# Kernel optimization log

Hardware: AMD Instinct MI355X
Metric: run time of the kernel (lower is better)

The kernel has to match this reference:

```python
import jax, jax.numpy as jnp
import numpy as np

T, Q, D, NH, L = 6, 300, 256, 8, 4
DH = D // NH
PC, PT = 2, 1
WT = T - 1
P = PC + WT * PT
DFF = 1024
SHAPES = [(128, 128), (64, 64), (32, 32), (16, 16)]
S_PER_FRAME = sum(h * w for h, w in SHAPES)


def _layer_norm(x, g, b, eps=1e-5):
    mu = jnp.mean(x, -1, keepdims=True)
    v = jnp.mean(jnp.square(x - mu), -1, keepdims=True)
    return (x - mu) * jax.lax.rsqrt(v + eps) * g + b


def _bilinear(vlh, loc, frame_pt, Hl, Wl):
    # vlh: [NH, T*Hl*Wl, DH]; loc: [TQ, NH, P, 2] normalized; frame_pt: np [TQ, P] int32
    x = loc[..., 0] * Wl - 0.5
    y = loc[..., 1] * Hl - 0.5
    x0 = jnp.floor(x)
    y0 = jnp.floor(y)
    fx = x - x0
    fy = y - y0
    x0 = x0.astype(jnp.int32)
    y0 = y0.astype(jnp.int32)
    fbase = (frame_pt[:, None, :] * np.int32(Hl * Wl)).astype(np.int32)  # [TQ,1,P]
    acc = 0.0
    for dy, wy in ((0, 1.0 - fy), (1, fy)):
        for dx, wx in ((0, 1.0 - fx), (1, fx)):
            xi = x0 + dx
            yi = y0 + dy
            ok = (xi >= 0) & (xi < Wl) & (yi >= 0) & (yi < Hl)
            idx = fbase + jnp.clip(yi, 0, Hl - 1) * Wl + jnp.clip(xi, 0, Wl - 1)  # [TQ,NH,P]
            g = jax.vmap(lambda v, i: v[i], in_axes=(0, 1), out_axes=0)(vlh, idx)  # [NH,TQ,P,DH]
            w = wy * wx * ok  # [TQ,NH,P]
            acc = acc + g * jnp.transpose(w, (1, 0, 2))[..., None]
    return acc  # [NH,TQ,P,DH]


def _forward(src, tgt_masks, query_pos, reference_points, src_valid_ratios,
             Wq, bq, Wk, bk, Wv, bv, Wo, bo, norm2_g, norm2_b,
             Wval, bval, Woff, boff, Watt, batt, Wout, bout, norm1_g, norm1_b,
             W1, b1, W2, b2, norm3_g, norm3_b,
             src_spatial_shapes, src_level_start_index):
    shapes = np.asarray(src_spatial_shapes)
    # ---- self-attention across frames (seq=T, batch=Q, as in nn.MultiheadAttention) ----
    qk_in = tgt_masks + query_pos  # [T,Q,D]
    qh = (qk_in @ Wq.T + bq).reshape(T, Q, NH, DH)
    kh = (qk_in @ Wk.T + bk).reshape(T, Q, NH, DH)
    vh = (tgt_masks @ Wv.T + bv).reshape(T, Q, NH, DH)
    logits = jnp.einsum('iqhd,jqhd->qhij', qh, kh) * (1.0 / np.sqrt(DH))
    attn = jax.nn.softmax(logits, -1)
    sa = jnp.einsum('qhij,jqhd->iqhd', attn, vh).reshape(T, Q, D) @ Wo.T + bo
    tgt = _layer_norm(tgt_masks + sa, norm2_g, norm2_b)  # [T,Q,D]

    tgt = tgt.reshape(T * Q, D)
    query = tgt + query_pos.reshape(T * Q, D)

    # ---- current-frame and temporal (same-instance) reference points ----
    ref = reference_points.reshape(T * Q, 2)
    vr0 = src_valid_ratios[0]  # [L,2]
    ref_curr = ref[:, None, :] * vr0[None]  # [TQ,L,2]
    others = np.array([[f for f in range(T) if f != t] for t in range(T)], np.int32)  # [T,WT]
    ref_oth = reference_points[others]  # [T,WT,Q,2]
    ref_oth = jnp.transpose(ref_oth, (0, 2, 1, 3)).reshape(T * Q, WT, 2)
    ref_temp = ref_oth[:, :, None, :] * vr0[None, None]  # [TQ,WT,L,2]

    fid = np.repeat(np.arange(T, dtype=np.int32), Q)  # [TQ]
    oth_fid = np.repeat(others, Q, axis=0)  # [TQ,WT]
    frame_pt = np.concatenate([np.tile(fid[:, None], (1, PC)), oth_fid], axis=1).astype(np.int32)  # [TQ,P]

    # ---- temporal multi-scale deformable cross-attention ----
    value = (src[0] @ Wval.T + bval).reshape(-1, NH, DH)  # [T*S,NH,DH]
    off = (query @ Woff.T + boff).reshape(T * Q, NH, L, P, 2)
    att = jax.nn.softmax((query @ Watt.T + batt).reshape(T * Q, NH, L * P), -1)
    att = att.reshape(T * Q, NH, L, P)

    out = jnp.zeros((T * Q, NH, DH), src.dtype)
    start = 0
    for l in range(L):
        Hl, Wl = int(shapes[l, 0]), int(shapes[l, 1])
        n = T * Hl * Wl
        vlh = value[start:start + n].transpose(1, 0, 2)  # [NH, T*Hl*Wl, DH]
        start += n
        bc = jnp.tile(ref_curr[:, l][:, None, :], (1, PC, 1))  # [TQ,PC,2]
        bt = ref_temp[:, :, l, :]  # [TQ,WT,2]
        base = jnp.concatenate([bc, bt], 1)[:, None]  # [TQ,1,P,2]
        loc = base + off[:, :, l] / jnp.array([Wl, Hl], jnp.float32)  # [TQ,NH,P,2]
        sampled = _bilinear(vlh, loc, frame_pt, Hl, Wl)  # [NH,TQ,P,DH]
        out = out + jnp.einsum('nqpd,qnp->qnd', sampled, att[:, :, l])
    cross = out.reshape(T * Q, D) @ Wout.T + bout
    tgt = _layer_norm(tgt + cross, norm1_g, norm1_b)

    # ---- FFN ----
    h = jax.nn.relu(tgt @ W1.T + b1)
    tgt = _layer_norm(tgt + h @ W2.T + b2, norm3_g, norm3_b)
    return tgt.reshape(T, Q, D)


def setup_inputs() -> dict:
    key = jax.random.key(0)
    ki = iter(jax.random.split(key, 48))

    def rn(shape, s=1.0):
        return jax.random.normal(next(ki), shape, jnp.float32) * s

    return {
        'src': rn((1, T * S_PER_FRAME, D)),
        'tgt_masks': rn((T, Q, D)),
        'query_pos': rn((T, Q, D), 0.5),
        'reference_points': jax.random.uniform(next(ki), (T, Q, 2), jnp.float32, 0.25, 0.75),
        'src_valid_ratios': jax.random.uniform(next(ki), (T, L, 2), jnp.float32, 0.9, 1.0),
        'src_spatial_shapes': jnp.array(SHAPES, jnp.int32),
        'src_level_start_index': jnp.array(np.cumsum([0] + [T * h * w for h, w in SHAPES[:-1]]), jnp.int32),
        'Wq': rn((D, D), 0.02), 'bq': jnp.zeros((D,)),
        'Wk': rn((D, D), 0.02), 'bk': jnp.zeros((D,)),
        'Wv': rn((D, D), 0.02), 'bv': jnp.zeros((D,)),
        'Wo': rn((D, D), 0.02), 'bo': jnp.zeros((D,)),
        'norm2_g': jnp.ones((D,)), 'norm2_b': jnp.zeros((D,)),
        'Wval': rn((D, D), 0.02), 'bval': jnp.zeros((D,)),
        'Woff': rn((NH * L * P * 2, D), 0.01), 'boff': rn((NH * L * P * 2,), 0.1),
        'Watt': rn((NH * L * P, D), 0.01), 'batt': jnp.zeros((NH * L * P,)),
        'Wout': rn((D, D), 0.02), 'bout': jnp.zeros((D,)),
        'norm1_g': jnp.ones((D,)), 'norm1_b': jnp.zeros((D,)),
        'W1': rn((DFF, D), 0.02), 'b1': jnp.zeros((DFF,)),
        'W2': rn((D, DFF), 0.02), 'b2': jnp.zeros((D,)),
        'norm3_g': jnp.ones((D,)), 'norm3_b': jnp.zeros((D,)),
    }


def reference(src, tgt_masks, query_pos, reference_points, src_valid_ratios,
              src_spatial_shapes, src_level_start_index,
              Wq, bq, Wk, bk, Wv, bv, Wo, bo, norm2_g, norm2_b,
              Wval, bval, Woff, boff, Watt, batt, Wout, bout, norm1_g, norm1_b,
              W1, b1, W2, b2, norm3_g, norm3_b):
    return _forward(src, tgt_masks, query_pos, reference_points, src_valid_ratios,
                    Wq, bq, Wk, bk, Wv, bv, Wo, bo, norm2_g, norm2_b,
                    Wval, bval, Woff, boff, Watt, batt, Wout, bout, norm1_g, norm1_b,
                    W1, b1, W2, b2, norm3_g, norm3_b,
                    src_spatial_shapes, src_level_start_index)
```

## Files before the change

kernel.cpp:

```cpp
#include <hip/hip_runtime.h>
#include <hip/hip_bf16.h>

#define T_ 6
#define Q_ 300
#define TQ 1800
#define D_ 256
#define NH_ 8
#define DH_ 32
#define L_ 4
#define P_ 7
#define DFF_ 1024
#define NV 130560
#define NVB 1020
#define QKVB 174

#define OW_VAL 0
#define OW_Q   65536
#define OW_K   131072
#define OW_V   196608
#define OW_O   262144
#define OW_OUT 327680
#define OW_OFF 393216
#define OW_ATT 507904
#define OW_1   565248
#define OW_2   827392
#define OW_TOT 1089536

typedef __attribute__((ext_vector_type(8))) short bf16x8;
typedef __attribute__((ext_vector_type(4))) float f32x4;
typedef __attribute__((ext_vector_type(8))) unsigned short u16x8;
typedef __attribute__((ext_vector_type(4))) unsigned short u16x4;

__device__ inline float bf2f(unsigned short s) {
    union { unsigned u; float f; } v; v.u = ((unsigned)s) << 16;
    return v.f;
}
__device__ inline unsigned short f2b_rn(float f) {
    __hip_bfloat16 h = __float2bfloat16(f);
    union { __hip_bfloat16 h; unsigned short u; } c; c.h = h; return c.u;
}

__global__ __launch_bounds__(256) void wcvt_kernel(
    const float* __restrict__ s0, const float* __restrict__ s1,
    const float* __restrict__ s2, const float* __restrict__ s3,
    const float* __restrict__ s4, const float* __restrict__ s5,
    const float* __restrict__ s6, const float* __restrict__ s7,
    const float* __restrict__ s8, const float* __restrict__ s9,
    unsigned short* __restrict__ dst)
{
    int idx4 = blockIdx.x * blockDim.x + threadIdx.x;
    const int total4 = OW_TOT / 4;
    for (; idx4 < total4; idx4 += gridDim.x * blockDim.x) {
        int e = idx4 * 4;
        const float* s; int off;
        if      (e < OW_Q)   { s = s0; off = e; }
        else if (e < OW_K)   { s = s1; off = e - OW_Q; }
        else if (e < OW_V)   { s = s2; off = e - OW_K; }
        else if (e < OW_O)   { s = s3; off = e - OW_V; }
        else if (e < OW_OUT) { s = s4; off = e - OW_O; }
        else if (e < OW_OFF) { s = s5; off = e - OW_OUT; }
        else if (e < OW_ATT) { s = s6; off = e - OW_OFF; }
        else if (e < OW_1)   { s = s7; off = e - OW_ATT; }
        else if (e < OW_2)   { s = s8; off = e - OW_1; }
        else                 { s = s9; off = e - OW_2; }
        f32x4 v = *(const f32x4*)(s + off);
        u16x4 o;
#pragma unroll
        for (int j = 0; j < 4; j++) o[j] = f2b_rn(v[j]);
        *(u16x4*)(dst + e) = o;
    }
}

__global__ __launch_bounds__(512, 4) void mega1_kernel(
    const float* __restrict__ A, const unsigned short* __restrict__ wbf,
    const float* __restrict__ bias,
    unsigned short* __restrict__ out,
    const float* __restrict__ tgtm, const float* __restrict__ qpos,
    const float* __restrict__ bq, const float* __restrict__ bk,
    const float* __restrict__ bv,
    float* __restrict__ qh, float* __restrict__ kh, float* __restrict__ vh)
{
    __shared__ unsigned short As[2][128 * 32];
    __shared__ unsigned short Bs[2][256 * 32];

    int tid = threadIdx.x;
    int wave = tid >> 6, lane = tid & 63;
    int r = lane & 15, g = lane >> 4;

    if (blockIdx.x < NVB) {
        const unsigned short* Wv = wbf + OW_VAL;
        int wm = wave >> 2, wn = wave & 3;
        int m0 = blockIdx.x * 128;

        int arow = tid >> 2, aq = tid & 3;
        const float* aptr = A + (size_t)(m0 + arow) * 256 + aq * 8;

        int dcol = (wave * 2) * 16 + (lane >> 2);
        int dkk = (lane & 3) * 8;

        f32x4 acc[4][4] = {};
        f32x4 aLo, aHi;

#define DMA_B(ks, buf) do { \
            const unsigned short* s0_ = Wv + (size_t)dcol * 256 + (ks) * 32 + dkk; \
            const unsigned short* s1_ = s0_ + 16 * 256; \
            __builtin_amdgcn_global_load_lds( \
                (const __attribute__((address_space(1))) void*)s0_, \
                (__attribute__((address_space(3))) void*)&Bs[buf][(wave * 2 + 0) * 512], 16, 0, 0); \
            __builtin_amdgcn_global_load_lds( \
                (const __attribute__((address_space(1))) void*)s1_, \
                (__attribute__((address_space(3))) void*)&Bs[buf][(wave * 2 + 1) * 512], 16, 0, 0); \
        } while (0)

        DMA_B(0, 0);
        aLo = *(const f32x4*)(aptr);
        aHi = *(const f32x4*)(aptr + 4);

#pragma unroll
        for (int ks = 0; ks < 8; ks++) {
            const int buf = ks & 1;
            u16x8 av;
#pragma unroll
            for (int j = 0; j < 4; j++) { av[j] = f2b_rn(aLo[j]); av[4 + j] = f2b_rn(aHi[j]); }
            *(u16x8*)&As[buf][arow * 32 + aq * 8] = av;

            asm volatile("s_waitcnt lgkmcnt(0)" ::: "memory");
            __builtin_amdgcn_s_barrier();
            __builtin_amdgcn_sched_barrier(0);

            if (ks < 7) {
                DMA_B(ks + 1, buf ^ 1);
                aLo = *(const f32x4*)(aptr + (ks + 1) * 32);
                aHi = *(const f32x4*)(aptr + (ks + 1) * 32 + 4);
            }

            bf16x8 af[4], bfr[4];
#pragma unroll
            for (int mi = 0; mi < 4; mi++)
                af[mi] = *(const bf16x8*)&As[buf][(wm * 64 + mi * 16 + r) * 32 + g * 8];
#pragma unroll
            for (int ni = 0; ni < 4; ni++)
                bfr[ni] = *(const bf16x8*)&Bs[buf][(wn * 64 + ni * 16 + r) * 32 + g * 8];
#pragma unroll
            for (int mi = 0; mi < 4; mi++)
#pragma unroll
                for (int ni = 0; ni < 4; ni++)
                    acc[mi][ni] = __builtin_amdgcn_mfma_f32_16x16x32_bf16(af[mi], bfr[ni], acc[mi][ni], 0, 0, 0);
        }
#undef DMA_B

#pragma unroll
        for (int ni = 0; ni < 4; ni++) {
            int col = wn * 64 + ni * 16 + r;
            float bv2 = bias[col];
#pragma unroll
            for (int mi = 0; mi < 4; mi++) {
#pragma unroll
                for (int rr = 0; rr < 4; rr++) {
                    int row = m0 + wm * 64 + mi * 16 + g * 4 + rr;
                    out[(size_t)row * 256 + col] = f2b_rn(acc[mi][ni][rr] + bv2);
                }
            }
        }
    } else {
        int b = blockIdx.x - NVB;
        int bmx = b % 29, by = b / 29;
        int wm = wave >> 2, wn = wave & 3;
        int m0 = bmx * 64 + wm * 32;
        int n0g = by * 128 + wn * 32;
        int seg = n0g >> 8;
        int n0 = n0g & 255;
        const unsigned short* Wp = wbf + (seg == 0 ? OW_Q : (seg == 1 ? OW_K : OW_V));
        const float* bp = (seg == 0) ? bq : (seg == 1) ? bk : bv;
        float* outp = (seg == 0) ? qh : (seg == 1) ? kh : vh;
        bool add2 = (seg < 2);

        f32x4 acc[2][2] = {};
#pragma unroll
        for (int kk = 0; kk < 256; kk += 32) {
            int kbase = kk + g * 8;
            bf16x8 af[2], wf[2];
#pragma unroll
            for (int mi = 0; mi < 2; mi++) {
                int row = m0 + mi * 16 + r; if (row >= TQ) row = TQ - 1;
                const float* ap = tgtm + (size_t)row * 256 + kbase;
                f32x4 lo = *(const f32x4*)ap, hi = *(const f32x4*)(ap + 4);
                if (add2) {
                    const float* ap2 = qpos + (size_t)row * 256 + kbase;
                    lo += *(const f32x4*)ap2; hi += *(const f32x4*)(ap2 + 4);
                }
#pragma unroll
                for (int j = 0; j < 4; j++) { af[mi][j] = (short)f2b_rn(lo[j]); af[mi][4 + j] = (short)f2b_rn(hi[j]); }
            }
#pragma unroll
            for (int ni = 0; ni < 2; ni++) {
                int col = n0 + ni * 16 + r;
                wf[ni] = *(const bf16x8*)&Wp[(size_t)col * 256 + kbase];
            }
#pragma unroll
            for (int mi = 0; mi < 2; mi++)
#pragma unroll
                for (int ni = 0; ni < 2; ni++)
                    acc[mi][ni] = __builtin_amdgcn_mfma_f32_16x16x32_bf16(af[mi], wf[ni], acc[mi][ni], 0, 0, 0);
        }
#pragma unroll
        for (int mi = 0; mi < 2; mi++)
#pragma unroll
            for (int ni = 0; ni < 2; ni++) {
                int col = n0 + ni * 16 + r;
                float bv2 = bp[col];
#pragma unroll
                for (int rr = 0; rr < 4; rr++) {
                    int row = m0 + mi * 16 + g * 4 + rr;
                    if (row < TQ) outp[(size_t)row * 256 + col] = acc[mi][ni][rr] + bv2;
                }
            }
    }
}

__global__ __launch_bounds__(256) void attn_wo_ln2_kernel(
    const float* __restrict__ qh, const float* __restrict__ kh,
    const float* __restrict__ vh, const float* __restrict__ tgtm,
    const float* __restrict__ qpos, const unsigned short* __restrict__ wbf,
    const float* __restrict__ bo, const float* __restrict__ n2g,
    const float* __restrict__ n2b,
    float* __restrict__ tgt1, float* __restrict__ query)
{
    int q = blockIdx.x;
    int tid = threadIdx.x;
    __shared__ float qs[T_][D_], ks_[T_][D_], vs[T_][D_];
    __shared__ unsigned short po[16][268];
    __shared__ float sa32[16][264];

#pragma unroll
    for (int i = 0; i < T_; i++) {
        size_t base = (size_t)(i * Q_ + q) * D_ + tid;
        qs[i][tid] = qh[base]; ks_[i][tid] = kh[base]; vs[i][tid] = vh[base];
    }
    __syncthreads();

    const float scale = 0.17677669529663687f;
    float lg[T_][T_];
#pragma unroll
    for (int i = 0; i < T_; i++)
#pragma unroll
        for (int j = 0; j < T_; j++) {
            float p = qs[i][tid] * ks_[j][tid];
#pragma unroll
            for (int m = 16; m >= 1; m >>= 1) p += __shfl_xor(p, m, 32);
            lg[i][j] = p * scale;
        }
#pragma unroll
    for (int i = 0; i < T_; i++) {
        float mx = lg[i][0];
#pragma unroll
        for (int j = 1; j < T_; j++) mx = fmaxf(mx, lg[i][j]);
        float w[T_]; float sum = 0.f;
#pragma unroll
        for (int j = 0; j < T_; j++) { w[j] = __expf(lg[i][j] - mx); sum += w[j]; }
        float inv = 1.f / sum;
        float a = 0.f;
#pragma unroll
        for (int j = 0; j < T_; j++) a += w[j] * inv * vs[j][tid];
        po[i][tid] = f2b_rn(a);
    }
#pragma unroll
    for (int i = T_; i < 16; i++) po[i][tid] = 0;
    __syncthreads();

    const unsigned short* Wo = wbf + OW_O;
    int wn = tid >> 6, lane = tid & 63;
    int r = lane & 15, g = lane >> 4;
    f32x4 acc[4] = {};
#pragma unroll
    for (int ksx = 0; ksx < 8; ksx++) {
        int kbase = ksx * 32 + g * 8;
        bf16x8 af = *(const bf16x8*)&po[r][kbase];
        bf16x8 bfr[4];
#pragma unroll
        for (int ni = 0; ni < 4; ni++)
            bfr[ni] = *(const bf16x8*)&Wo[(size_t)(wn * 64 + ni * 16 + r) * 256 + kbase];
#pragma unroll
        for (int ni = 0; ni < 4; ni++)
            acc[ni] = __builtin_amdgcn_mfma_f32_16x16x32_bf16(af, bfr[ni], acc[ni], 0, 0, 0);
    }
#pragma unroll
    for (int ni = 0; ni < 4; ni++) {
        int col = wn * 64 + ni * 16 + r;
#pragma unroll
        for (int rr = 0; rr < 4; rr++) {
            int row = g * 4 + rr;
            if (row < T_)
                sa32[row][col] = acc[ni][rr] + bo[col] + tgtm[(size_t)(row * Q_ + q) * 256 + col];
        }
    }
    __syncthreads();

    int rl = tid >> 3, l8 = tid & 7;
    if (rl < T_) {
        float s = 0.f, s2 = 0.f;
#pragma unroll
        for (int c = 0; c < 256; c += 8) {
            float v = sa32[rl][c + l8];
            s += v; s2 += v * v;
        }
#pragma unroll
        for (int m = 4; m >= 1; m >>= 1) { s += __shfl_xor(s, m, 64); s2 += __shfl_xor(s2, m, 64); }
        float mu = s * (1.f / 256.f);
        float var = s2 * (1.f / 256.f) - mu * mu;
        float rs = rsqrtf(var + 1e-5f);
        size_t grow = (size_t)(rl * Q_ + q) * 256;
#pragma unroll
        for (int c = 0; c < 256; c += 8) {
            int cc = c + l8;
            float y = (sa32[rl][cc] - mu) * rs * n2g[cc] + n2b[cc];
            tgt1[grow + cc] = y;
            query[grow + cc] = y + qpos[grow + cc];
        }
    }
}

__global__ __launch_bounds__(256) void offatt_kernel(
    const float* __restrict__ query, const unsigned short* __restrict__ wbf,
    const float* __restrict__ boff, const float* __restrict__ batt,
    float* __restrict__ offb, float* __restrict__ attl)
{
    int wave = threadIdx.x >> 6;
    int lane = threadIdx.x & 63;
    int wm = wave >> 1, wn = wave & 1;
    int m0 = blockIdx.x * 64 + wm * 32;
    int n0g = blockIdx.y * 64 + wn * 32;
    int seg = (n0g >= 448);
    int n0 = seg ? (n0g - 448) : n0g;
    int Nloc = seg ? 224 : 448;
    const unsigned short* W = wbf + (seg ? OW_ATT : OW_OFF);
    const float* bias = seg ? batt : boff;
    float* out = seg ? attl : offb;
    int r = lane & 15, g = lane >> 4;

    f32x4 acc[2][2] = {};
#pragma unroll
    for (int kk = 0; kk < 256; kk += 32) {
        int kbase = kk + g * 8;
        bf16x8 af[2], wf[2];
#pragma unroll
        for (int mi = 0; mi < 2; mi++) {
            int row = m0 + mi * 16 + r; if (row >= TQ) row = TQ - 1;
            const float* ap = query + (size_t)row * 256 + kbase;
            f32x4 lo = *(const f32x4*)ap, hi = *(const f32x4*)(ap + 4);
#pragma unroll
            for (int j = 0; j < 4; j++) { af[mi][j] = (short)f2b_rn(lo[j]); af[mi][4 + j] = (short)f2b_rn(hi[j]); }
        }
#pragma unroll
        for (int ni = 0; ni < 2; ni++) {
            int col = n0 + ni * 16 + r; if (col >= Nloc) col = Nloc - 1;
            wf[ni] = *(const bf16x8*)&W[(size_t)col * 256 + kbase];
        }
#pragma unroll
        for (int mi = 0; mi < 2; mi++)
#pragma unroll
            for (int ni = 0; ni < 2; ni++)
                acc[mi][ni] = __builtin_amdgcn_mfma_f32_16x16x32_bf16(af[mi], wf[ni], acc[mi][ni], 0, 0, 0);
    }
#pragma unroll
    for (int mi = 0; mi < 2; mi++)
#pragma unroll
        for (int ni = 0; ni < 2; ni++) {
            int col = n0 + ni * 16 + r;
            if (col < Nloc) {
                float bv2 = bias[col];
#pragma unroll
                for (int rr = 0; rr < 4; rr++) {
                    int row = m0 + mi * 16 + g * 4 + rr;
                    if (row < TQ) out[(size_t)row * Nloc + col] = acc[mi][ni][rr] + bv2;
                }
            }
        }
}

__global__ __launch_bounds__(256) void sample_kernel(
    const unsigned short* __restrict__ value, const float* __restrict__ attl,
    const float* __restrict__ off, const float* __restrict__ refp,
    const float* __restrict__ vr, float* __restrict__ out)
{
    int q = blockIdx.x;
    int tid = threadIdx.x;
    int d = tid & 31, h = tid >> 5;
    int t = q / Q_, qq = q - t * Q_;

    __shared__ float aw[NH_][28], ofx[NH_][28], ofy[NH_][28];

    float lgv = (d < 28) ? attl[(size_t)q * 224 + h * 28 + d] : -1e30f;
    float mx = lgv;
#pragma unroll
    for (int m = 16; m >= 1; m >>= 1) mx = fmaxf(mx, __shfl_xor(mx, m, 32));
    float e = (d < 28) ? __expf(lgv - mx) : 0.f;
    float s = e;
#pragma unroll
    for (int m = 16; m >= 1; m >>= 1) s += __shfl_xor(s, m, 32);
    if (d < 28) {
        aw[h][d] = e / s;
        ofx[h][d] = off[(size_t)q * 448 + h * 56 + d * 2 + 0];
        ofy[h][d] = off[(size_t)q * 448 + h * 56 + d * 2 + 1];
    }
    __syncthreads();

    const int WLs[4] = {128, 64, 32, 16};
    const int LST[4] = {0, 98304, 122880, 129024};

    float acc = 0.f;
#pragma unroll
    for (int l = 0; l < L_; l++) {
        const int Wl = WLs[l], Hl = WLs[l];
        const int lst = LST[l];
        float vrx = vr[l * 2 + 0], vry = vr[l * 2 + 1];
#pragma unroll
        for (int p = 0; p < P_; p++) {
            int f = (p < 2) ? t : (((p - 2) < t) ? (p - 2) : (p - 1));
            float rx = refp[(size_t)(f * Q_ + qq) * 2 + 0];
            float ry = refp[(size_t)(f * Q_ + qq) * 2 + 1];
            int ip = l * 7 + p;
            float x = rx * vrx * (float)Wl + ofx[h][ip] - 0.5f;
            float y = ry * vry * (float)Hl + ofy[h][ip] - 0.5f;
            float x0f = floorf(x), y0f = floorf(y);
            float fx = x - x0f, fy = y - y0f;
            int x0 = (int)x0f, y0 = (int)y0f;
            int fbase = lst + f * Hl * Wl;
            float a = aw[h][ip];
#pragma unroll
            for (int dy = 0; dy < 2; dy++) {
                int yi = y0 + dy;
                float wy = dy ? fy : 1.f - fy;
                int yc = min(max(yi, 0), Hl - 1);
                bool oky = (yi >= 0) && (yi < Hl);
#pragma unroll
                for (int dx = 0; dx < 2; dx++) {
                    int xi = x0 + dx;
                    float wx = dx ? fx : 1.f - fx;
                    int xc = min(max(xi, 0), Wl - 1);
                    bool ok = oky && (xi >= 0) && (xi < Wl);
                    float v = bf2f(value[((size_t)(fbase + yc * Wl + xc)) * D_ + h * DH_ + d]);
                    acc += a * (ok ? (wy * wx) : 0.f) * v;
                }
            }
        }
    }
    out[(size_t)q * D_ + tid] = acc;
}

__global__ __launch_bounds__(256) void tail_kernel(
    const float* __restrict__ samp, const unsigned short* __restrict__ wbf,
    const float* __restrict__ bout, const float* __restrict__ tgt1,
    const float* __restrict__ n1g, const float* __restrict__ n1b,
    const float* __restrict__ b1, const float* __restrict__ b2,
    const float* __restrict__ n3g, const float* __restrict__ n3b,
    float* __restrict__ dout)
{
    __shared__ float c32[16][264];
    __shared__ float t232[16][264];
    __shared__ unsigned short t2bf[16][268];
    __shared__ unsigned short hbf[16][1036];

    int tid = threadIdx.x;
    int wn = tid >> 6, lane = tid & 63;
    int r = lane & 15, g = lane >> 4;
    int m0 = blockIdx.x * 16;

    const unsigned short* Wout = wbf + OW_OUT;
    const unsigned short* W1 = wbf + OW_1;
    const unsigned short* W2 = wbf + OW_2;

    {
        f32x4 acc[4] = {};
        int row = m0 + r; if (row >= TQ) row = TQ - 1;
#pragma unroll
        for (int ksx = 0; ksx < 8; ksx++) {
            int kbase = ksx * 32 + g * 8;
            const float* ap = samp + (size_t)row * 256 + kbase;
            f32x4 lo = *(const f32x4*)ap, hi = *(const f32x4*)(ap + 4);
            bf16x8 af;
#pragma unroll
            for (int j = 0; j < 4; j++) { af[j] = (short)f2b_rn(lo[j]); af[4 + j] = (short)f2b_rn(hi[j]); }
            bf16x8 bfr[4];
#pragma unroll
            for (int ni = 0; ni < 4; ni++)
                bfr[ni] = *(const bf16x8*)&Wout[(size_t)(wn * 64 + ni * 16 + r) * 256 + kbase];
#pragma unroll
            for (int ni = 0; ni < 4; ni++)
                acc[ni] = __builtin_amdgcn_mfma_f32_16x16x32_bf16(af, bfr[ni], acc[ni], 0, 0, 0);
        }
#pragma unroll
        for (int ni = 0; ni < 4; ni++) {
            int col = wn * 64 + ni * 16 + r;
            float bv = bout[col];
#pragma unroll
            for (int rr = 0; rr < 4; rr++) {
                int rowl = g * 4 + rr;
                int grow = m0 + rowl;
                float res = (grow < TQ) ? tgt1[(size_t)grow * 256 + col] : 0.f;
                c32[rowl][col] = acc[ni][rr] + bv + res;
            }
        }
    }
    __syncthreads();

    if (tid < 128) {
        int rl = tid >> 3, l8 = tid & 7;
        float s = 0.f, s2 = 0.f;
#pragma unroll
        for (int c = 0; c < 256; c += 8) {
            float v = c32[rl][c + l8];
            s += v; s2 += v * v;
        }
#pragma unroll
        for (int m = 4; m >= 1; m >>= 1) { s += __shfl_xor(s, m, 64); s2 += __shfl_xor(s2, m, 64); }
        float mu = s * (1.f / 256.f);
        float var = s2 * (1.f / 256.f) - mu * mu;
        float rs = rsqrtf(var + 1e-5f);
#pragma unroll
        for (int c = 0; c < 256; c += 8) {
            int cc = c + l8;
            float y = (c32[rl][cc] - mu) * rs * n1g[cc] + n1b[cc];
            t232[rl][cc] = y;
            t2bf[rl][cc] = f2b_rn(y);
        }
    }
    __syncthreads();

    {
        f32x4 acc[16] = {};
#pragma unroll
        for (int ksx = 0; ksx < 8; ksx++) {
            int kbase = ksx * 32 + g * 8;
            bf16x8 af = *(const bf16x8*)&t2bf[r][kbase];
#pragma unroll
            for (int ni = 0; ni < 16; ni++) {
                bf16x8 bfr = *(const bf16x8*)&W1[(size_t)(wn * 256 + ni * 16 + r) * 256 + kbase];
                acc[ni] = __builtin_amdgcn_mfma_f32_16x16x32_bf16(af, bfr, acc[ni], 0, 0, 0);
            }
        }
#pragma unroll
        for (int ni = 0; ni < 16; ni++) {
            int col = wn * 256 + ni * 16 + r;
            float bv = b1[col];
#pragma unroll
            for (int rr = 0; rr < 4; rr++) {
                int rowl = g * 4 + rr;
                hbf[rowl][col] = f2b_rn(fmaxf(acc[ni][rr] + bv, 0.f));
            }
        }
    }
    __syncthreads();

    {
        f32x4 acc[4] = {};
#pragma unroll
        for (int ksx = 0; ksx < 32; ksx++) {
            int kbase = ksx * 32 + g * 8;
            bf16x8 af = *(const bf16x8*)&hbf[r][kbase];
#pragma unroll
            for (int ni = 0; ni < 4; ni++) {
                bf16x8 bfr = *(const bf16x8*)&W2[(size_t)(wn * 64 + ni * 16 + r) * 1024 + kbase];
                acc[ni] = __builtin_amdgcn_mfma_f32_16x16x32_bf16(af, bfr, acc[ni], 0, 0, 0);
            }
        }
#pragma unroll
        for (int ni = 0; ni < 4; ni++) {
            int col = wn * 64 + ni * 16 + r;
            float bv = b2[col];
#pragma unroll
            for (int rr = 0; rr < 4; rr++) {
                int rowl = g * 4 + rr;
                c32[rowl][col] = acc[ni][rr] + bv + t232[rowl][col];
            }
        }
    }
    __syncthreads();

    if (tid < 128) {
        int rl = tid >> 3, l8 = tid & 7;
        int grow = m0 + rl;
        if (grow < TQ) {
            float s = 0.f, s2 = 0.f;
#pragma unroll
            for (int c = 0; c < 256; c += 8) {
                float v = c32[rl][c + l8];
                s += v; s2 += v * v;
            }
#pragma unroll
            for (int m = 4; m >= 1; m >>= 1) { s += __shfl_xor(s, m, 64); s2 += __shfl_xor(s2, m, 64); }
            float mu = s * (1.f / 256.f);
            float var = s2 * (1.f / 256.f) - mu * mu;
            float rs = rsqrtf(var + 1e-5f);
#pragma unroll
            for (int c = 0; c < 256; c += 8) {
                int cc = c + l8;
                dout[(size_t)grow * 256 + cc] = (c32[rl][cc] - mu) * rs * n3g[cc] + n3b[cc];
            }
        }
    }
}

extern "C" void kernel_launch(void* const* d_in, const int* in_sizes, int n_in,
                              void* d_out, int out_size, void* d_ws, size_t ws_size,
                              hipStream_t stream) {
    const float* src  = (const float*)d_in[0];
    const float* tgtm = (const float*)d_in[1];
    const float* qpos = (const float*)d_in[2];
    const float* refp = (const float*)d_in[3];
    const float* vr   = (const float*)d_in[4];
    const float* Wq = (const float*)d_in[7];  const float* bq = (const float*)d_in[8];
    const float* Wk = (const float*)d_in[9];  const float* bk = (const float*)d_in[10];
    const float* Wv = (const float*)d_in[11]; const float* bv = (const float*)d_in[12];
    const float* Wo = (const float*)d_in[13]; const float* bo = (const float*)d_in[14];
    const float* n2g = (const float*)d_in[15]; const float* n2b = (const float*)d_in[16];
    const float* Wval = (const float*)d_in[17]; const float* bval = (const float*)d_in[18];
    const float* Woff = (const float*)d_in[19]; const float* boff = (const float*)d_in[20];
    const float* Watt = (const float*)d_in[21]; const float* batt = (const float*)d_in[22];
    const float* Wout = (const float*)d_in[23]; const float* bout = (const float*)d_in[24];
    const float* n1g = (const float*)d_in[25]; const float* n1b = (const float*)d_in[26];
    const float* W1 = (const float*)d_in[27]; const float* b1 = (const float*)d_in[28];
    const float* W2 = (const float*)d_in[29]; const float* b2 = (const float*)d_in[30];
    const float* n3g = (const float*)d_in[31]; const float* n3b = (const float*)d_in[32];

    char* ws = (char*)d_ws;
    size_t o = 0;
    auto alloc = [&](size_t bytes) -> void* {
        void* p = ws + o; o += (bytes + 255) & ~(size_t)255; return p;
    };
    unsigned short* value = (unsigned short*)alloc((size_t)NV * D_ * 2);
    unsigned short* wbf   = (unsigned short*)alloc((size_t)OW_TOT * 2);
    float* qh     = (float*)alloc((size_t)TQ * D_ * 4);
    float* kh     = (float*)alloc((size_t)TQ * D_ * 4);
    float* vh     = (float*)alloc((size_t)TQ * D_ * 4);
    float* tgt1   = (float*)alloc((size_t)TQ * D_ * 4);
    float* query  = (float*)alloc((size_t)TQ * D_ * 4);
    float* offb   = (float*)alloc((size_t)TQ * 448 * 4);
    float* attl   = (float*)alloc((size_t)TQ * 224 * 4);
    float* samp   = (float*)alloc((size_t)TQ * D_ * 4);

    const int MT = (TQ + 63) / 64;

    wcvt_kernel<<<dim3((OW_TOT / 4 + 255) / 256), dim3(256), 0, stream>>>(
        Wval, Wq, Wk, Wv, Wo, Wout, Woff, Watt, W1, W2, wbf);

    mega1_kernel<<<dim3(NVB + QKVB), dim3(512), 0, stream>>>(
        src, wbf, bval, value, tgtm, qpos, bq, bk, bv, qh, kh, vh);

    attn_wo_ln2_kernel<<<dim3(Q_), dim3(256), 0, stream>>>(
        qh, kh, vh, tgtm, qpos, wbf, bo, n2g, n2b, tgt1, query);

    offatt_kernel<<<dim3(MT, 11), dim3(256), 0, stream>>>(query, wbf, boff, batt, offb, attl);

    sample_kernel<<<dim3(TQ), dim3(256), 0, stream>>>(value, attl, offb, refp, vr, samp);

    tail_kernel<<<dim3((TQ + 15) / 16), dim3(256), 0, stream>>>(
        samp, wbf, bout, tgt1, n1g, n1b, b1, b2, n3g, n3b, (float*)d_out);
}
```

Measured before the change: 178.7 us.

## Replace LDS-staged value projection GEMM with register-pipelined direct global loads

Measured after the change: 235.6 us. 1.32x slower.

```diff
diff --git a/kernel.cpp b/kernel.cpp
--- a/kernel.cpp
+++ b/kernel.cpp
@@ -71,7 +71,7 @@
     }
 }
 
-__global__ __launch_bounds__(512, 4) void mega1_kernel(
+__global__ __launch_bounds__(512) void mega1_kernel(
     const float* __restrict__ A, const unsigned short* __restrict__ wbf,
     const float* __restrict__ bias,
     unsigned short* __restrict__ out,
@@ -80,9 +80,6 @@
     const float* __restrict__ bv,
     float* __restrict__ qh, float* __restrict__ kh, float* __restrict__ vh)
 {
-    __shared__ unsigned short As[2][128 * 32];
-    __shared__ unsigned short Bs[2][256 * 32];
-
     int tid = threadIdx.x;
     int wave = tid >> 6, lane = tid & 63;
     int r = lane & 15, g = lane >> 4;
@@ -90,74 +87,76 @@
     if (blockIdx.x < NVB) {
         const unsigned short* Wv = wbf + OW_VAL;
         int wm = wave >> 2, wn = wave & 3;
-        int m0 = blockIdx.x * 128;
-
-        int arow = tid >> 2, aq = tid & 3;
-        const float* aptr = A + (size_t)(m0 + arow) * 256 + aq * 8;
-
-        int dcol = (wave * 2) * 16 + (lane >> 2);
-        int dkk = (lane & 3) * 8;
-
+        int m0 = blockIdx.x * 128 + wm * 64;
+        int n0 = wn * 64;
+
+        const float* aptr[4];
+        const unsigned short* bptr[4];
+#pragma unroll
+        for (int i = 0; i < 4; i++) {
+            aptr[i] = A + (size_t)(m0 + i * 16 + r) * 256 + g * 8;
+            bptr[i] = Wv + (size_t)(n0 + i * 16 + r) * 256 + g * 8;
+        }
+
+        f32x4 aLo0[4], aHi0[4]; bf16x8 bF0[4];
+        f32x4 aLo1[4], aHi1[4]; bf16x8 bF1[4];
+        f32x4 aLo2[4], aHi2[4]; bf16x8 bF2[4];
         f32x4 acc[4][4] = {};
-        f32x4 aLo, aHi;
-
-#define DMA_B(ks, buf) do { \
-            const unsigned short* s0_ = Wv + (size_t)dcol * 256 + (ks) * 32 + dkk; \
-            const unsigned short* s1_ = s0_ + 16 * 256; \
-            __builtin_amdgcn_global_load_lds( \
-                (const __attribute__((address_space(1))) void*)s0_, \
-                (__attribute__((address_space(3))) void*)&Bs[buf][(wave * 2 + 0) * 512], 16, 0, 0); \
-            __builtin_amdgcn_global_load_lds( \
-                (const __attribute__((address_space(1))) void*)s1_, \
-                (__attribute__((address_space(3))) void*)&Bs[buf][(wave * 2 + 1) * 512], 16, 0, 0); \
+
+#define ISSUE(S, kk) do { \
+        _Pragma("unroll") \
+        for (int i = 0; i < 4; i++) { \
+            aLo##S[i] = *(const f32x4*)(aptr[i] + (kk)); \
+            aHi##S[i] = *(const f32x4*)(aptr[i] + (kk) + 4); \
+            bF##S[i]  = *(const bf16x8*)(bptr[i] + (kk)); \
+        } } while (0)
+
+#define COMPUTE(S) do { \
+        bf16x8 af[4]; \
+        _Pragma("unroll") \
+        for (int i = 0; i < 4; i++) { \
+            _Pragma("unroll") \
+            for (int j = 0; j < 4; j++) { \
+                af[i][j] = (short)f2b_rn(aLo##S[i][j]); \
+                af[i][4 + j] = (short)f2b_rn(aHi##S[i][j]); \
+            } \
+        } \
+        _Pragma("unroll") \
+        for (int mi = 0; mi < 4; mi++) \
+            _Pragma("unroll") \
+            for (int ni = 0; ni < 4; ni++) \
+                acc[mi][ni] = __builtin_amdgcn_mfma_f32_16x16x32_bf16(af[mi], bF##S[ni], acc[mi][ni], 0, 0, 0); \
         } while (0)
 
-        DMA_B(0, 0);
-        aLo = *(const f32x4*)(aptr);
-        aHi = *(const f32x4*)(aptr + 4);
-
-#pragma unroll
-        for (int ks = 0; ks < 8; ks++) {
-            const int buf = ks & 1;
-            u16x8 av;
-#pragma unroll
-            for (int j = 0; j < 4; j++) { av[j] = f2b_rn(aLo[j]); av[4 + j] = f2b_rn(aHi[j]); }
-            *(u16x8*)&As[buf][arow * 32 + aq * 8] = av;
-
-            asm volatile("s_waitcnt lgkmcnt(0)" ::: "memory");
-            __builtin_amdgcn_s_barrier();
-            __builtin_amdgcn_sched_barrier(0);
-
-            if (ks < 7) {
-                DMA_B(ks + 1, buf ^ 1);
-                aLo = *(const f32x4*)(aptr + (ks + 1) * 32);
-                aHi = *(const f32x4*)(aptr + (ks + 1) * 32 + 4);
-            }
-
-            bf16x8 af[4], bfr[4];
-#pragma unroll
-            for (int mi = 0; mi < 4; mi++)
-                af[mi] = *(const bf16x8*)&As[buf][(wm * 64 + mi * 16 + r) * 32 + g * 8];
-#pragma unroll
-            for (int ni = 0; ni < 4; ni++)
-                bfr[ni] = *(const bf16x8*)&Bs[buf][(wn * 64 + ni * 16 + r) * 32 + g * 8];
-#pragma unroll
-            for (int mi = 0; mi < 4; mi++)
-#pragma unroll
-                for (int ni = 0; ni < 4; ni++)
-                    acc[mi][ni] = __builtin_amdgcn_mfma_f32_16x16x32_bf16(af[mi], bfr[ni], acc[mi][ni], 0, 0, 0);
-        }
-#undef DMA_B
+        ISSUE(0, 0); ISSUE(1, 32); ISSUE(2, 64);
+        __builtin_amdgcn_sched_barrier(0);
+        COMPUTE(0); ISSUE(0, 96);
+        __builtin_amdgcn_sched_barrier(0);
+        COMPUTE(1); ISSUE(1, 128);
+        __builtin_amdgcn_sched_barrier(0);
+        COMPUTE(2); ISSUE(2, 160);
+        __builtin_amdgcn_sched_barrier(0);
+        COMPUTE(0); ISSUE(0, 192);
+        __builtin_amdgcn_sched_barrier(0);
+        COMPUTE(1); ISSUE(1, 224);
+        __builtin_amdgcn_sched_barrier(0);
+        COMPUTE(2);
+        __builtin_amdgcn_sched_barrier(0);
+        COMPUTE(0);
+        __builtin_amdgcn_sched_barrier(0);
+        COMPUTE(1);
+#undef ISSUE
+#undef COMPUTE
 
 #pragma unroll
         for (int ni = 0; ni < 4; ni++) {
-            int col = wn * 64 + ni * 16 + r;
+            int col = n0 + ni * 16 + r;
             float bv2 = bias[col];
 #pragma unroll
             for (int mi = 0; mi < 4; mi++) {
 #pragma unroll
                 for (int rr = 0; rr < 4; rr++) {
-                    int row = m0 + wm * 64 + mi * 16 + g * 4 + rr;
+                    int row = m0 + mi * 16 + g * 4 + rr;
                     out[(size_t)row * 256 + col] = f2b_rn(acc[mi][ni][rr] + bv2);
                 }
             }
```
